# Optimization experiments

Hardware: AMD Instinct MI355X
Metric: run time of the kernel (lower is better)

Reference implementation:

```python
import jax, jax.numpy as jnp
import numpy as np

DROPOUT_P = 0.2
HEAD_SIZE = 64
EMBED = 1024


def setup_inputs() -> dict:
    key = jax.random.key(0)
    kx, kk, kq, kv = jax.random.split(key, 4)
    B, T = 4, 4096
    x = jax.random.normal(kx, (B, T, EMBED), dtype=jnp.float32)
    # torch Linear(embed, head, bias=False): y = x @ W.T with W [head, embed].
    # We store W_* as [embed, head] so projection is x @ W.
    scale = 1.0 / np.sqrt(EMBED)
    Wk = jax.random.uniform(kk, (EMBED, HEAD_SIZE), jnp.float32, -scale, scale)
    Wq = jax.random.uniform(kq, (EMBED, HEAD_SIZE), jnp.float32, -scale, scale)
    Wv = jax.random.uniform(kv, (EMBED, HEAD_SIZE), jnp.float32, -scale, scale)
    return {"x": x, "Wk": Wk, "Wq": Wq, "Wv": Wv}


def reference(x, Wk, Wq, Wv):
    # Projections: [B,T,E] @ [E,H] -> [B,T,H]
    k = jnp.einsum("bte,eh->bth", x, Wk)
    q = jnp.einsum("bte,eh->bth", x, Wq)
    v = jnp.einsum("bte,eh->bth", x, Wv)
    # Raw scaled scores, NO softmax: [B,T,T]
    w = jnp.einsum("bqh,bkh->bqk", q, k) * (HEAD_SIZE ** -0.5)
    # Dropout (training mode, inverted scaling) with a fixed key.
    keep = jax.random.bernoulli(jax.random.key(42), 1.0 - DROPOUT_P, w.shape)
    w = jnp.where(keep, w / (1.0 - DROPOUT_P), 0.0)
    # Weighted V sum: [B,T,T] @ [B,T,H] -> [B,T,H]
    return jnp.einsum("bqk,bkh->bqh", w, v)
```

## Files before the change

kernel.cpp:

```cpp
#include <hip/hip_runtime.h>


#define TB 4
#define TT 4096
#define TE 1024
#define TH 64
#define COMB_SCALE 0.15625f

typedef __bf16 bf16x8 __attribute__((ext_vector_type(8)));
typedef __bf16 bf16x4 __attribute__((ext_vector_type(4)));
typedef float  f32x4  __attribute__((ext_vector_type(4)));

#define ROTL(x, d) __builtin_amdgcn_alignbit((x), (x), 32u - (d))

__device__ __forceinline__ unsigned tf_bits(unsigned j) {
  const unsigned ks1 = 42u;
  const unsigned ks2 = 0x1BD11BDAu ^ 42u;
  unsigned x0 = 0u, x1 = j + ks1;
#define TF_RND(d) { x0 += x1; x1 = ROTL(x1, (d)); x1 ^= x0; }
  TF_RND(13u) TF_RND(15u) TF_RND(26u) TF_RND(6u)
  x0 += ks1; x1 += ks2 + 1u;
  TF_RND(17u) TF_RND(29u) TF_RND(16u) TF_RND(24u)
  x0 += ks2; x1 += 0u + 2u;
  TF_RND(13u) TF_RND(15u) TF_RND(26u) TF_RND(6u)
  x0 += 0u;  x1 += ks1 + 3u;
  TF_RND(17u) TF_RND(29u) TF_RND(16u) TF_RND(24u)
  x0 += ks1; x1 += ks2 + 4u;
  TF_RND(13u) TF_RND(15u) TF_RND(26u) TF_RND(6u)
  x0 += ks2; x1 += 0u + 5u;
#undef TF_RND
  return x0 ^ x1;
}

__device__ __forceinline__ bool tf_keep(unsigned j) {
  return tf_bits(j) < 3435974144u;
}

__global__ __launch_bounds__(256)
void prep_wt(const float* __restrict__ Wq, const float* __restrict__ Wk,
             const float* __restrict__ Wv, __bf16* __restrict__ WT)
{
  __shared__ float lds[64][65];
  const int wi = blockIdx.x >> 4;
  const int k0 = (blockIdx.x & 15) * 64;
  const float* W = (wi == 0) ? Wq : ((wi == 1) ? Wk : Wv);
  const int tid = threadIdx.x;
#pragma unroll
  for (int it = 0; it < 16; ++it) {
    const int idx = tid + it * 256;
    lds[idx >> 6][idx & 63] = W[(size_t)(k0 + (idx >> 6)) * TH + (idx & 63)];
  }
  __syncthreads();
#pragma unroll
  for (int it = 0; it < 16; ++it) {
    const int idx = tid + it * 256;
    const int n = idx >> 6, kk = idx & 63;
    WT[(size_t)(wi * TH + n) * TE + k0 + kk] = (__bf16)lds[kk][n];
  }
}

__global__ __launch_bounds__(256)
void proj_mfma(const float* __restrict__ x, const __bf16* __restrict__ WT,
               __bf16* __restrict__ qs, __bf16* __restrict__ ks,
               __bf16* __restrict__ vT)
{
  const int tid = threadIdx.x;
  const int w  = tid >> 6, l = tid & 63;
  const int l4 = l >> 4,  lm = l & 15;
  const int rh = w >> 1,  ch = w & 1;
  const int R  = blockIdx.x * 32 + rh * 16;

  const float*  xr = x  + (size_t)(R + lm) * TE;
  const __bf16* wt = WT + (size_t)(ch * 96 + lm) * TE;

  f32x4 acc[6];
#pragma unroll
  for (int t = 0; t < 6; ++t) acc[t] = (f32x4){0.f, 0.f, 0.f, 0.f};

  for (int k0 = 0; k0 < TE; k0 += 32) {
    const float4 u0 = *reinterpret_cast<const float4*>(xr + k0 + l4 * 8);
    const float4 u1 = *reinterpret_cast<const float4*>(xr + k0 + l4 * 8 + 4);
    bf16x8 am;
    am[0] = (__bf16)u0.x; am[1] = (__bf16)u0.y;
    am[2] = (__bf16)u0.z; am[3] = (__bf16)u0.w;
    am[4] = (__bf16)u1.x; am[5] = (__bf16)u1.y;
    am[6] = (__bf16)u1.z; am[7] = (__bf16)u1.w;
    bf16x8 bn[6];
#pragma unroll
    for (int t = 0; t < 6; ++t)
      bn[t] = *reinterpret_cast<const bf16x8*>(wt + (size_t)t * 16 * TE + k0 + l4 * 8);
#pragma unroll
    for (int t = 0; t < 6; ++t)
      acc[t] = __builtin_amdgcn_mfma_f32_16x16x32_bf16(am, bn[t], acc[t], 0, 0, 0);
  }

  const int row0 = R + l4 * 4;
#pragma unroll
  for (int t = 0; t < 6; ++t) {
    const int n = ch * 96 + t * 16 + lm;
    if (n < TH) {
#pragma unroll
      for (int r = 0; r < 4; ++r)
        qs[(size_t)(row0 + r) * TH + n] = (__bf16)(acc[t][r] * COMB_SCALE);
    } else if (n < 2 * TH) {
#pragma unroll
      for (int r = 0; r < 4; ++r)
        ks[(size_t)(row0 + r) * TH + (n - TH)] = (__bf16)acc[t][r];
    } else {
      bf16x4 vv;
#pragma unroll
      for (int r = 0; r < 4; ++r) vv[r] = (__bf16)acc[t][r];
      const int bb = row0 >> 12, trow = row0 & (TT - 1);
      *reinterpret_cast<bf16x4*>(
          vT + ((size_t)(bb * TH + (n - 2 * TH)) * TT + trow)) = vv;
    }
  }
}

__global__ __launch_bounds__(512, 8)
void attn_mfma(const __bf16* __restrict__ qs,
               const __bf16* __restrict__ ks,
               const __bf16* __restrict__ vT,
               float* __restrict__ out)
{
  __shared__ __bf16 S_lds[8][16 * 64];
  __shared__ float  Oex[4][16][TH + 4];

  const int tid = threadIdx.x;
  const int w   = tid >> 6;
  const int l   = tid & 63;
  const int l4  = l >> 4;
  const int lm  = l & 15;

  const int b     = blockIdx.x >> 8;
  const int qt16  = blockIdx.x & 255;
  const int qrow0 = qt16 * 16;
  const int kv0   = w * (TT / 8);

  const __bf16* qb = qs + ((size_t)b * TT + qrow0) * TH;
  const bf16x8 qf0 = *reinterpret_cast<const bf16x8*>(qb + (size_t)lm * TH + l4 * 8);
  const bf16x8 qf1 = *reinterpret_cast<const bf16x8*>(qb + (size_t)lm * TH + 32 + l4 * 8);

  const __bf16* kbp = ks + (size_t)b * TT * TH;
  const __bf16* vbp = vT + (size_t)b * TH * TT;

  f32x4 o_acc[4];
#pragma unroll
  for (int t = 0; t < 4; ++t) o_acc[t] = (f32x4){0.f, 0.f, 0.f, 0.f};

  const unsigned base0 = ((unsigned)(b * TT) + (unsigned)qrow0 + (unsigned)(l4 * 4)) * (unsigned)TT;
  const unsigned sw = (unsigned)((lm & 7) << 3);

  for (int kb = kv0; kb < kv0 + TT / 8; kb += 64) {
    bf16x8 kf[4][2];
#pragma unroll
    for (int t = 0; t < 4; ++t) {
      const __bf16* kr = kbp + (size_t)(kb + t * 16 + lm) * TH;
#pragma unroll
      for (int s = 0; s < 2; ++s)
        kf[t][s] = *reinterpret_cast<const bf16x8*>(kr + s * 32 + l4 * 8);
    }

    f32x4 sa[4];
#pragma unroll
    for (int t = 0; t < 4; ++t) {
      f32x4 c = {0.f, 0.f, 0.f, 0.f};
      c = __builtin_amdgcn_mfma_f32_16x16x32_bf16(qf0, kf[t][0], c, 0, 0, 0);
      c = __builtin_amdgcn_mfma_f32_16x16x32_bf16(qf1, kf[t][1], c, 0, 0, 0);
      sa[t] = c;
    }

    bf16x8 vf[4][2];
#pragma unroll
    for (int t = 0; t < 4; ++t) {
      const __bf16* vr = vbp + (size_t)(t * 16 + lm) * TT + kb;
#pragma unroll
      for (int s = 0; s < 2; ++s)
        vf[t][s] = *reinterpret_cast<const bf16x8*>(vr + s * 32 + l4 * 8);
    }

    const unsigned jcol = (unsigned)kb + (unsigned)lm;
#pragma unroll
    for (int t = 0; t < 4; ++t) {
#pragma unroll
      for (int r = 0; r < 4; ++r) {
        const unsigned j = base0 + (unsigned)(r * TT) + jcol + (unsigned)(t * 16);
        const float svv = tf_keep(j) ? sa[t][r] : 0.0f;
        const int row = l4 * 4 + r;
        const int col = t * 16 + lm;
        S_lds[w][row * 64 + (col ^ ((row & 7) << 3))] = (__bf16)svv;
      }
    }

    const bf16x8 af0 = *reinterpret_cast<const bf16x8*>(
        &S_lds[w][lm * 64 + ((unsigned)(l4 * 8) ^ sw)]);
    const bf16x8 af1 = *reinterpret_cast<const bf16x8*>(
        &S_lds[w][lm * 64 + ((unsigned)(32 + l4 * 8) ^ sw)]);

#pragma unroll
    for (int t = 0; t < 4; ++t) {
      o_acc[t] = __builtin_amdgcn_mfma_f32_16x16x32_bf16(af0, vf[t][0], o_acc[t], 0, 0, 0);
      o_acc[t] = __builtin_amdgcn_mfma_f32_16x16x32_bf16(af1, vf[t][1], o_acc[t], 0, 0, 0);
    }
  }

  if (w >= 4) {
#pragma unroll
    for (int t = 0; t < 4; ++t)
#pragma unroll
      for (int r = 0; r < 4; ++r)
        Oex[w - 4][l4 * 4 + r][t * 16 + lm] = o_acc[t][r];
  }
  __syncthreads();
  if (w < 4) {
#pragma unroll
    for (int t = 0; t < 4; ++t)
#pragma unroll
      for (int r = 0; r < 4; ++r)
        o_acc[t][r] += Oex[w][l4 * 4 + r][t * 16 + lm];
  }
  __syncthreads();
  if (w == 2 || w == 3) {
#pragma unroll
    for (int t = 0; t < 4; ++t)
#pragma unroll
      for (int r = 0; r < 4; ++r)
        Oex[w - 2][l4 * 4 + r][t * 16 + lm] = o_acc[t][r];
  }
  __syncthreads();
  if (w < 2) {
#pragma unroll
    for (int t = 0; t < 4; ++t)
#pragma unroll
      for (int r = 0; r < 4; ++r)
        o_acc[t][r] += Oex[w][l4 * 4 + r][t * 16 + lm];
  }
  __syncthreads();
  if (w == 1) {
#pragma unroll
    for (int t = 0; t < 4; ++t)
#pragma unroll
      for (int r = 0; r < 4; ++r)
        Oex[0][l4 * 4 + r][t * 16 + lm] = o_acc[t][r];
  }
  __syncthreads();
  if (w == 0) {
    float* outb = out + ((size_t)b * TT + qrow0) * TH;
#pragma unroll
    for (int t = 0; t < 4; ++t)
#pragma unroll
      for (int r = 0; r < 4; ++r) {
        const int row = l4 * 4 + r, col = t * 16 + lm;
        outb[(size_t)row * TH + col] = o_acc[t][r] + Oex[0][row][col];
      }
  }
}

extern "C" void kernel_launch(void* const* d_in, const int* in_sizes, int n_in,
                              void* d_out, int out_size, void* d_ws, size_t ws_size,
                              hipStream_t stream) {
  const float* x  = (const float*)d_in[0];
  const float* Wk = (const float*)d_in[1];
  const float* Wq = (const float*)d_in[2];
  const float* Wv = (const float*)d_in[3];
  float* outp = (float*)d_out;

  const size_t SZ = (size_t)TB * TT * TH;
  __bf16* q_ws  = (__bf16*)d_ws;
  __bf16* k_ws  = q_ws + SZ;
  __bf16* vT_ws = k_ws + SZ;
  __bf16* WT_ws = vT_ws + SZ;

  prep_wt<<<dim3(48), dim3(256), 0, stream>>>(Wq, Wk, Wv, WT_ws);
  proj_mfma<<<dim3(TB * TT / 32), dim3(256), 0, stream>>>(
      x, WT_ws, q_ws, k_ws, vT_ws);
  attn_mfma<<<dim3(TB * (TT / 16)), dim3(512), 0, stream>>>(
      q_ws, k_ws, vT_ws, outp);
}
```

Measured before the change: 219.7 us.

## Precompute dropout mask bits in projection kernel and consume packed mask in attention

Moves the Threefry dropout-mask generation out of the attention kernel into the projection kernel, where each thread computes 16 keep bits per K-step and writes a packed 32-bit word to a workspace buffer. The attention kernel then loads one word per 64-column tile and applies the mask with bitwise AND instead of hashing inline. This aims to hide the integer-heavy RNG behind the memory-bound projection and to shorten the attention loop's ALU path. The cost is 32 MB of extra mask traffic (write plus read) and a heavier projection kernel, which also gets a launch-bounds occupancy hint.

```diff
diff --git a/kernel.cpp b/kernel.cpp
--- a/kernel.cpp
+++ b/kernel.cpp
@@ -32,8 +32,8 @@
   return x0 ^ x1;
 }
 
-__device__ __forceinline__ bool tf_keep(unsigned j) {
-  return tf_bits(j) < 3435974144u;
+__device__ __forceinline__ unsigned tf_keep(unsigned j) {
+  return tf_bits(j) < 3435974144u ? 1u : 0u;
 }
 
 __global__ __launch_bounds__(256)
@@ -59,10 +59,10 @@
   }
 }
 
-__global__ __launch_bounds__(256)
+__global__ __launch_bounds__(256, 2)
 void proj_mfma(const float* __restrict__ x, const __bf16* __restrict__ WT,
                __bf16* __restrict__ qs, __bf16* __restrict__ ks,
-               __bf16* __restrict__ vT)
+               __bf16* __restrict__ vT, unsigned* __restrict__ mask)
 {
   const int tid = threadIdx.x;
   const int w  = tid >> 6, l = tid & 63;
@@ -72,6 +72,8 @@
 
   const float*  xr = x  + (size_t)(R + lm) * TE;
   const __bf16* wt = WT + (size_t)(ch * 96 + lm) * TE;
+
+  const unsigned gtid = (unsigned)(blockIdx.x * 256 + tid);
 
   f32x4 acc[6];
 #pragma unroll
@@ -92,6 +94,25 @@
 #pragma unroll
     for (int t = 0; t < 6; ++t)
       acc[t] = __builtin_amdgcn_mfma_f32_16x16x32_bf16(am, bn[t], acc[t], 0, 0, 0);
+
+    {
+      const unsigned d  = gtid + (unsigned)(k0 >> 5) * 131072u;
+      const unsigned A  = d >> 12;
+      const unsigned mw = (d >> 9) & 7u;
+      const unsigned ms = (d >> 6) & 7u;
+      const unsigned ml = d & 63u;
+      const unsigned bq = A >> 8, qt = A & 255u;
+      const unsigned jb = ((bq << 12) + qt * 16u + (ml >> 4) * 4u) * 4096u +
+                          mw * 512u + ms * 64u + (ml & 15u);
+      unsigned m = 0u;
+#pragma unroll
+      for (int t = 0; t < 4; ++t)
+#pragma unroll
+        for (int r = 0; r < 4; ++r)
+          m |= tf_keep(jb + (unsigned)(r << 12) + (unsigned)(t << 4))
+               << (t * 4 + r);
+      mask[d] = m;
+    }
   }
 
   const int row0 = R + l4 * 4;
@@ -121,6 +142,7 @@
 void attn_mfma(const __bf16* __restrict__ qs,
                const __bf16* __restrict__ ks,
                const __bf16* __restrict__ vT,
+               const unsigned* __restrict__ mask,
                float* __restrict__ out)
 {
   __shared__ __bf16 S_lds[8][16 * 64];
@@ -143,22 +165,25 @@
 
   const __bf16* kbp = ks + (size_t)b * TT * TH;
   const __bf16* vbp = vT + (size_t)b * TH * TT;
+  const unsigned* mkp = mask + (((size_t)blockIdx.x * 8 + w) * 8) * 64 + l;
 
   f32x4 o_acc[4];
 #pragma unroll
   for (int t = 0; t < 4; ++t) o_acc[t] = (f32x4){0.f, 0.f, 0.f, 0.f};
 
-  const unsigned base0 = ((unsigned)(b * TT) + (unsigned)qrow0 + (unsigned)(l4 * 4)) * (unsigned)TT;
   const unsigned sw = (unsigned)((lm & 7) << 3);
 
-  for (int kb = kv0; kb < kv0 + TT / 8; kb += 64) {
+  for (int s = 0; s < 8; ++s) {
+    const int kb = kv0 + s * 64;
+    const unsigned mdw = mkp[s * 64];
+
     bf16x8 kf[4][2];
 #pragma unroll
     for (int t = 0; t < 4; ++t) {
       const __bf16* kr = kbp + (size_t)(kb + t * 16 + lm) * TH;
 #pragma unroll
-      for (int s = 0; s < 2; ++s)
-        kf[t][s] = *reinterpret_cast<const bf16x8*>(kr + s * 32 + l4 * 8);
+      for (int ss = 0; ss < 2; ++ss)
+        kf[t][ss] = *reinterpret_cast<const bf16x8*>(kr + ss * 32 + l4 * 8);
     }
 
     f32x4 sa[4];
@@ -175,20 +200,20 @@
     for (int t = 0; t < 4; ++t) {
       const __bf16* vr = vbp + (size_t)(t * 16 + lm) * TT + kb;
 #pragma unroll
-      for (int s = 0; s < 2; ++s)
-        vf[t][s] = *reinterpret_cast<const bf16x8*>(vr + s * 32 + l4 * 8);
-    }
-
-    const unsigned jcol = (unsigned)kb + (unsigned)lm;
+      for (int ss = 0; ss < 2; ++ss)
+        vf[t][ss] = *reinterpret_cast<const bf16x8*>(vr + ss * 32 + l4 * 8);
+    }
+
 #pragma unroll
     for (int t = 0; t < 4; ++t) {
 #pragma unroll
       for (int r = 0; r < 4; ++r) {
-        const unsigned j = base0 + (unsigned)(r * TT) + jcol + (unsigned)(t * 16);
-        const float svv = tf_keep(j) ? sa[t][r] : 0.0f;
+        const unsigned keepneg = 0u - ((mdw >> (t * 4 + r)) & 1u);
+        const unsigned sb = __float_as_uint(sa[t][r]) & keepneg;
         const int row = l4 * 4 + r;
         const int col = t * 16 + lm;
-        S_lds[w][row * 64 + (col ^ ((row & 7) << 3))] = (__bf16)svv;
+        S_lds[w][row * 64 + (col ^ ((row & 7) << 3))] =
+            (__bf16)__uint_as_float(sb);
       }
     }
 
@@ -270,10 +295,11 @@
   __bf16* k_ws  = q_ws + SZ;
   __bf16* vT_ws = k_ws + SZ;
   __bf16* WT_ws = vT_ws + SZ;
+  unsigned* mask_ws = (unsigned*)(WT_ws + 192 * TE);
 
   prep_wt<<<dim3(48), dim3(256), 0, stream>>>(Wq, Wk, Wv, WT_ws);
   proj_mfma<<<dim3(TB * TT / 32), dim3(256), 0, stream>>>(
-      x, WT_ws, q_ws, k_ws, vT_ws);
+      x, WT_ws, q_ws, k_ws, vT_ws, mask_ws);
   attn_mfma<<<dim3(TB * (TT / 16)), dim3(512), 0, stream>>>(
-      q_ws, k_ws, vT_ws, outp);
-}
+      q_ws, k_ws, vT_ws, mask_ws, outp);
+}
```

New measurement: 300.1 us. 36.6% more time.
